# Kernel tuning notes

Hardware: AMD Instinct MI355X
Metric: run time of the kernel (lower is better)

## Reference

```python
import math
import jax, jax.numpy as jnp
import numpy as np

N_NODES = 50000
N_EDGES = 800000
F_IN = 512
HID = 64
N_CLS = 64
NITER = 10


def setup_inputs() -> dict:
    key = jax.random.key(0)
    k = jax.random.split(key, 6)
    x = jax.random.normal(k[0], (N_NODES, F_IN), jnp.float32)
    edge_index = jax.random.randint(k[1], (2, N_EDGES), 0, N_NODES, jnp.int64)
    W1 = jax.random.normal(k[2], (F_IN, HID), jnp.float32) / np.sqrt(F_IN)
    b1 = jnp.zeros((HID,), jnp.float32)
    W2 = jax.random.normal(k[3], (HID, N_CLS), jnp.float32) / np.sqrt(HID)
    b2 = jnp.zeros((N_CLS,), jnp.float32)
    halt_w = jax.random.normal(k[4], (N_CLS,), jnp.float32) / np.sqrt(N_CLS)
    # reset_parameters: bias = log((1/(niter+1)) / (1 - 1/(niter+1)))
    b = math.log((1.0 / (NITER + 1)) / (1.0 - 1.0 / (NITER + 1)))
    halt_b = jnp.full((1,), b, jnp.float32)
    return {"x": x, "edge_index": edge_index, "W1": W1, "b1": b1,
            "W2": W2, "b2": b2, "halt_w": halt_w, "halt_b": halt_b}


def reference(x, edge_index, W1, b1, W2, b2, halt_w, halt_b):
    N = x.shape[0]
    # MLP (eval mode: dropout is identity)
    h = jnp.maximum(x @ W1 + b1, 0.0)
    local = h @ W2 + b2                      # [N, C] local predictions
    # GCN normalization with self-loops (eval: no edge dropout)
    loops = jnp.arange(N, dtype=edge_index.dtype)
    row = jnp.concatenate([edge_index[0], loops])
    col = jnp.concatenate([edge_index[1], loops])
    deg = jnp.zeros((N,), x.dtype).at[row].add(1.0)
    dis = jnp.where(deg > 0, jax.lax.rsqrt(jnp.maximum(deg, 1.0)), 0.0)
    norm = dis[row] * dis[col]               # [E+N]

    def step(carry, _):
        prop, steps, sum_h, cont, xacc = carry
        old = prop
        msg = norm[:, None] * prop[row]                       # gather + scale
        prop = jax.ops.segment_sum(msg, col, num_segments=N)  # scatter-add
        hh = jax.nn.sigmoid(prop @ halt_w + halt_b[0])        # [N]
        prob = (sum_h + hh < 0.99) & cont
        pf = prob.astype(x.dtype)
        steps = steps + pf
        sum_h = sum_h + pf * hh
        cond = prob & (steps < NITER)
        p = jnp.where(cond, sum_h, 1.0 - sum_h)
        xacc = xacc + (prop * p[:, None] + old * (1.0 - p)[:, None]) * cont.astype(x.dtype)[:, None]
        cont = cont & prob
        return (prop, steps, sum_h, cont, xacc), None

    init = (local, jnp.ones((N,), x.dtype), jnp.zeros((N,), x.dtype),
            jnp.ones((N,), bool), jnp.zeros_like(local))
    (prop, steps, sum_h, cont, xacc), _ = jax.lax.scan(step, init, None, length=NITER)
    out = xacc / steps[:, None]
    return jax.nn.log_softmax(out, axis=1), steps, 1.0 - sum_h
```

## Files before the change

### kernel.cpp

```cpp
#include <hip/hip_runtime.h>
#include <hip/hip_bf16.h>

#define F_IN 512
#define NC 64
#define NITER 10
#define BM 128
#define BK 64

__global__ __launch_bounds__(256) void init_state_kernel(
    float* __restrict__ steps, float* __restrict__ sumh, int* __restrict__ cont,
    int* __restrict__ rowptr, int N, int E) {
  int i = blockIdx.x * blockDim.x + threadIdx.x;
  if (i < N) { steps[i] = 1.0f; sumh[i] = 0.0f; cont[i] = 1; }
  if (i == 0) rowptr[N] = E;
}

__global__ __launch_bounds__(256) void mlp_kernel(
    const float* __restrict__ x, const float* __restrict__ W1,
    const float* __restrict__ b1, const float* __restrict__ W2,
    const float* __restrict__ b2, float* __restrict__ out, int N) {
  __shared__ float xT[BK * 128];
  __shared__ float ws[BK * NC];
  const int tid  = threadIdx.x;
  const int brow = blockIdx.x * BM;
  const int r0 = (tid >> 4) * 8;
  const int c0 = (tid & 15) * 4;

  float acc[8][4];
#pragma unroll
  for (int j = 0; j < 4; ++j) {
    float bv = b1[c0 + j];
#pragma unroll
    for (int i = 0; i < 8; ++i) acc[i][j] = bv;
  }

  for (int kt = 0; kt < F_IN; kt += BK) {
#pragma unroll
    for (int q = 0; q < 8; ++q) {
      int fidx = q * 256 + tid;
      int row = fidx >> 4, kq = fidx & 15;
      int gr = brow + row; if (gr >= N) gr = N - 1;
      float4 v = *reinterpret_cast<const float4*>(&x[(size_t)gr * F_IN + kt + kq * 4]);
      float vv[4] = {v.x, v.y, v.z, v.w};
#pragma unroll
      for (int j = 0; j < 4; ++j) {
        int kk = kq * 4 + j;
        xT[kk * 128 + (row ^ (kk & 28))] = vv[j];
      }
    }
#pragma unroll
    for (int q = 0; q < 4; ++q) {
      int fidx = q * 256 + tid;
      int row = fidx >> 4, kq = fidx & 15;
      *reinterpret_cast<float4*>(&ws[row * NC + kq * 4]) =
          *reinterpret_cast<const float4*>(&W1[(size_t)(kt + row) * NC + kq * 4]);
    }
    __syncthreads();
#pragma unroll 4
    for (int k = 0; k < BK; ++k) {
      float4 xa = *reinterpret_cast<const float4*>(&xT[k * 128 + (r0 ^ (k & 28))]);
      float4 xb = *reinterpret_cast<const float4*>(&xT[k * 128 + ((r0 + 4) ^ (k & 28))]);
      float4 wv = *reinterpret_cast<const float4*>(&ws[k * NC + c0]);
      float xr[8] = {xa.x, xa.y, xa.z, xa.w, xb.x, xb.y, xb.z, xb.w};
      float wr[4] = {wv.x, wv.y, wv.z, wv.w};
#pragma unroll
      for (int i = 0; i < 8; ++i)
#pragma unroll
        for (int j = 0; j < 4; ++j) acc[i][j] = fmaf(xr[i], wr[j], acc[i][j]);
    }
    __syncthreads();
  }

#pragma unroll
  for (int i = 0; i < 8; ++i)
#pragma unroll
    for (int j = 0; j < 4; ++j) {
      int kk = c0 + j;
      int r  = r0 + i;
      xT[kk * 128 + (r ^ (kk & 28))] = fmaxf(acc[i][j], 0.0f);
    }
#pragma unroll
  for (int q = 0; q < 4; ++q) {
    int fidx = q * 256 + tid;
    int row = fidx >> 4, kq = fidx & 15;
    *reinterpret_cast<float4*>(&ws[row * NC + kq * 4]) =
        *reinterpret_cast<const float4*>(&W2[(size_t)row * NC + kq * 4]);
  }
  float acc2[8][4];
#pragma unroll
  for (int j = 0; j < 4; ++j) {
    float bv = b2[c0 + j];
#pragma unroll
    for (int i = 0; i < 8; ++i) acc2[i][j] = bv;
  }
  __syncthreads();
#pragma unroll 4
  for (int k = 0; k < NC; ++k) {
    float4 xa = *reinterpret_cast<const float4*>(&xT[k * 128 + (r0 ^ (k & 28))]);
    float4 xb = *reinterpret_cast<const float4*>(&xT[k * 128 + ((r0 + 4) ^ (k & 28))]);
    float4 wv = *reinterpret_cast<const float4*>(&ws[k * NC + c0]);
    float xr[8] = {xa.x, xa.y, xa.z, xa.w, xb.x, xb.y, xb.z, xb.w};
    float wr[4] = {wv.x, wv.y, wv.z, wv.w};
#pragma unroll
    for (int i = 0; i < 8; ++i)
#pragma unroll
      for (int j = 0; j < 4; ++j) acc2[i][j] = fmaf(xr[i], wr[j], acc2[i][j]);
  }
#pragma unroll
  for (int i = 0; i < 8; ++i) {
    int gr = brow + r0 + i;
    if (gr < N) {
      float4 o = make_float4(acc2[i][0], acc2[i][1], acc2[i][2], acc2[i][3]);
      *reinterpret_cast<float4*>(&out[(size_t)gr * NC + c0]) = o;
    }
  }
}

__global__ __launch_bounds__(256) void hist_kernel(
    const int* __restrict__ ei, int* __restrict__ deg_i,
    int* __restrict__ indeg, int E) {
  int e = blockIdx.x * blockDim.x + threadIdx.x;
  if (e < E) {
    atomicAdd(&deg_i[ei[e]], 1);
    atomicAdd(&indeg[ei[E + e]], 1);
  }
}

__global__ __launch_bounds__(256) void dis_kernel(
    const int* __restrict__ deg_i, float* __restrict__ dis, int N) {
  int i = blockIdx.x * blockDim.x + threadIdx.x;
  if (i < N) dis[i] = 1.0f / sqrtf((float)(deg_i[i] + 1));
}

__global__ __launch_bounds__(256) void scan_sum_kernel(
    const int* __restrict__ indeg, int* __restrict__ bsum, int N) {
  __shared__ int sm[256];
  int tid = threadIdx.x;
  int i = blockIdx.x * 256 + tid;
  sm[tid] = (i < N) ? indeg[i] : 0;
  __syncthreads();
  for (int s = 128; s > 0; s >>= 1) {
    if (tid < s) sm[tid] += sm[tid + s];
    __syncthreads();
  }
  if (tid == 0) bsum[blockIdx.x] = sm[0];
}

__global__ __launch_bounds__(256) void scan_bsum_kernel(int* __restrict__ bsum, int nb) {
  __shared__ int sm[256];
  int tid = threadIdx.x;
  int v = (tid < nb) ? bsum[tid] : 0;
  sm[tid] = v;
  __syncthreads();
  for (int s = 1; s < 256; s <<= 1) {
    int t = (tid >= s) ? sm[tid - s] : 0;
    __syncthreads();
    sm[tid] += t;
    __syncthreads();
  }
  if (tid < nb) bsum[tid] = sm[tid] - v;
}

__global__ __launch_bounds__(256) void scan_final_kernel(
    const int* __restrict__ indeg, const int* __restrict__ bsum,
    int* __restrict__ rowptr, int N) {
  __shared__ int sm[256];
  int tid = threadIdx.x;
  int i = blockIdx.x * 256 + tid;
  int v = (i < N) ? indeg[i] : 0;
  sm[tid] = v;
  __syncthreads();
  for (int s = 1; s < 256; s <<= 1) {
    int t = (tid >= s) ? sm[tid - s] : 0;
    __syncthreads();
    sm[tid] += t;
    __syncthreads();
  }
  if (i < N) rowptr[i] = bsum[blockIdx.x] + sm[tid] - v;
}

__global__ __launch_bounds__(256) void scatter_kernel(
    const int* __restrict__ ei, const int* __restrict__ rowptr,
    int* __restrict__ cursor, const float* __restrict__ dis,
    int2* __restrict__ csr, int E) {
  int e = blockIdx.x * blockDim.x + threadIdx.x;
  if (e < E) {
    int s = ei[e];
    int c = ei[E + e];
    int pos = rowptr[c] + atomicAdd(&cursor[c], 1);
    csr[pos] = make_int2(s, __float_as_int(dis[s] * dis[c]));
  }
}

__global__ __launch_bounds__(256) void prop_step_kernel(
    const float* __restrict__ prop, float* __restrict__ prop_new,
    const int2* __restrict__ csr, const int* __restrict__ rowptr,
    const float* __restrict__ dis, const float* __restrict__ hw,
    const float* __restrict__ hb, float* __restrict__ steps,
    float* __restrict__ sumh, int* __restrict__ cont,
    float* __restrict__ xacc, int N) {
  int wid = (int)((blockIdx.x * blockDim.x + threadIdx.x) >> 6);
  if (wid >= N) return;
  int lane = threadIdx.x & 63;
  size_t rowoff = (size_t)wid * NC + lane;

  float oldv = prop[rowoff];
  float dc = dis[wid];
  int beg = __builtin_amdgcn_readfirstlane(rowptr[wid]);
  int end = __builtin_amdgcn_readfirstlane(rowptr[wid + 1]);

  float a[8];
  a[0] = dc * dc * oldv;
#pragma unroll
  for (int u = 1; u < 8; ++u) a[u] = 0.0f;
  int i = beg;
  for (; i + 8 <= end; i += 8) {
    int2 e[8];
#pragma unroll
    for (int u = 0; u < 8; ++u) e[u] = csr[i + u];
#pragma unroll
    for (int u = 0; u < 8; ++u)
      a[u] = fmaf(__int_as_float(e[u].y), prop[(size_t)e[u].x * NC + lane], a[u]);
  }
  for (; i < end; ++i) {
    int2 e0 = csr[i];
    a[0] = fmaf(__int_as_float(e0.y), prop[(size_t)e0.x * NC + lane], a[0]);
  }
  float acc = ((a[0] + a[1]) + (a[2] + a[3])) + ((a[4] + a[5]) + (a[6] + a[7]));
  prop_new[rowoff] = acc;

  float z = acc * hw[lane];
#pragma unroll
  for (int off = 32; off > 0; off >>= 1) z += __shfl_xor(z, off);
  z += hb[0];
  float hh = 1.0f / (1.0f + expf(-z));

  float st = steps[wid], sh = sumh[wid];
  int ct = cont[wid];
  bool prob = ((sh + hh) < 0.99f) && (ct != 0);
  float pf = prob ? 1.0f : 0.0f;
  st += pf;
  sh += pf * hh;
  bool cond = prob && (st < (float)NITER);
  float pp = cond ? sh : (1.0f - sh);
  float ctf = ct ? 1.0f : 0.0f;
  xacc[rowoff] += (acc * pp + oldv * (1.0f - pp)) * ctf;
  if (lane == 0) { steps[wid] = st; sumh[wid] = sh; cont[wid] = prob ? 1 : 0; }
}

__global__ __launch_bounds__(256) void final_kernel(
    const float* __restrict__ xacc, const float* __restrict__ steps,
    const float* __restrict__ sumh, float* __restrict__ out0,
    float* __restrict__ out1, float* __restrict__ out2, int N) {
  int wid = (int)((blockIdx.x * blockDim.x + threadIdx.x) >> 6);
  if (wid >= N) return;
  int lane = threadIdx.x & 63;
  float st = steps[wid];
  float v = xacc[(size_t)wid * NC + lane] / st;
  float m = v;
#pragma unroll
  for (int off = 32; off > 0; off >>= 1) m = fmaxf(m, __shfl_xor(m, off));
  float e = expf(v - m);
  float s = e;
#pragma unroll
  for (int off = 32; off > 0; off >>= 1) s += __shfl_xor(s, off);
  out0[(size_t)wid * NC + lane] = v - m - logf(s);
  if (lane == 0) { out1[wid] = st; out2[wid] = 1.0f - sumh[wid]; }
}

extern "C" void kernel_launch(void* const* d_in, const int* in_sizes, int n_in,
                              void* d_out, int out_size, void* d_ws, size_t ws_size,
                              hipStream_t stream) {
  const float* x      = (const float*)d_in[0];
  const int*   ei     = (const int*)d_in[1];
  const float* W1     = (const float*)d_in[2];
  const float* b1     = (const float*)d_in[3];
  const float* W2     = (const float*)d_in[4];
  const float* b2     = (const float*)d_in[5];
  const float* halt_w = (const float*)d_in[6];
  const float* halt_b = (const float*)d_in[7];

  const int N = in_sizes[0] / F_IN;
  const int E = in_sizes[1] / 2;

  char* p = (char*)d_ws;
  auto alloc = [&](size_t bytes) {
    void* r = (void*)p;
    p += (bytes + 255) & ~(size_t)255;
    return r;
  };
  float* propA  = (float*)alloc((size_t)N * NC * 4);
  float* propB  = (float*)alloc((size_t)N * NC * 4);
  float* xacc   = (float*)alloc((size_t)N * NC * 4);
  int2*  csr    = (int2*)alloc((size_t)E * 8);
  int*   rowptr = (int*)alloc((size_t)(N + 1) * 4);
  int*   deg_i  = (int*)alloc((size_t)N * 4);
  int*   indeg  = (int*)alloc((size_t)N * 4);
  int*   cursor = (int*)alloc((size_t)N * 4);
  float* dis    = (float*)alloc((size_t)N * 4);
  float* steps  = (float*)alloc((size_t)N * 4);
  float* sumh   = (float*)alloc((size_t)N * 4);
  int*   cont   = (int*)alloc((size_t)N * 4);
  int*   bsum   = (int*)alloc(1024);

  hipMemsetAsync(deg_i,  0, (size_t)N * 4, stream);
  hipMemsetAsync(indeg,  0, (size_t)N * 4, stream);
  hipMemsetAsync(cursor, 0, (size_t)N * 4, stream);
  hipMemsetAsync(xacc,   0, (size_t)N * NC * 4, stream);

  const int nbN = (N + 255) / 256;
  const int nbE = (E + 255) / 256;
  const int nbM = (N + BM - 1) / BM;

  init_state_kernel<<<nbN, 256, 0, stream>>>(steps, sumh, cont, rowptr, N, E);
  mlp_kernel<<<nbM, 256, 0, stream>>>(x, W1, b1, W2, b2, propA, N);
  hist_kernel<<<nbE, 256, 0, stream>>>(ei, deg_i, indeg, E);
  dis_kernel<<<nbN, 256, 0, stream>>>(deg_i, dis, N);
  scan_sum_kernel<<<nbN, 256, 0, stream>>>(indeg, bsum, N);
  scan_bsum_kernel<<<1, 256, 0, stream>>>(bsum, nbN);
  scan_final_kernel<<<nbN, 256, 0, stream>>>(indeg, bsum, rowptr, N);
  scatter_kernel<<<nbE, 256, 0, stream>>>(ei, rowptr, cursor, dis, csr, E);

  float* out0 = (float*)d_out;
  float* out1 = out0 + (size_t)N * NC;
  float* out2 = out1 + N;

  const float* cur = propA;
  float* nxt = propB;
  const int nbW = (N + 3) / 4;
  for (int it = 0; it < NITER; ++it) {
    prop_step_kernel<<<nbW, 256, 0, stream>>>(cur, nxt, csr, rowptr, dis,
                                              halt_w, halt_b, steps, sumh,
                                              cont, xacc, N);
    const float* t = nxt; nxt = (float*)cur; cur = t;
  }
  final_kernel<<<nbW, 256, 0, stream>>>(xacc, steps, sumh, out0, out1, out2, N);
}
```

Measured before the change: 578.6 us.

## Fuse propagation iterations into one cooperative persistent kernel with grid sync

Replaces the ten per-iteration propagation launches and the final kernel with a single cooperative kernel. Each of 1024 blocks owns 49 nodes, keeps their halting state and accumulator in shared memory, and uses grid.sync between iterations. The goal is to remove launch overhead and global round-trips for steps, sumh, cont and xacc, at the cost of grid-wide barriers and a fixed grid size. It also halves the MLP tile height to 64 rows so more blocks are launched. If the cooperative launch fails, it falls back to the old path.

```diff
diff --git a/kernel.cpp b/kernel.cpp
--- a/kernel.cpp
+++ b/kernel.cpp
@@ -1,11 +1,16 @@
 #include <hip/hip_runtime.h>
 #include <hip/hip_bf16.h>
+#include <hip/hip_cooperative_groups.h>
+
+namespace cg = cooperative_groups;
 
 #define F_IN 512
 #define NC 64
 #define NITER 10
-#define BM 128
+#define BM 64
 #define BK 64
+#define G_COOP 1024
+#define NPB 49
 
 __global__ __launch_bounds__(256) void init_state_kernel(
     float* __restrict__ steps, float* __restrict__ sumh, int* __restrict__ cont,
@@ -19,24 +24,24 @@
     const float* __restrict__ x, const float* __restrict__ W1,
     const float* __restrict__ b1, const float* __restrict__ W2,
     const float* __restrict__ b2, float* __restrict__ out, int N) {
-  __shared__ float xT[BK * 128];
+  __shared__ float xT[BK * BM];
   __shared__ float ws[BK * NC];
   const int tid  = threadIdx.x;
   const int brow = blockIdx.x * BM;
-  const int r0 = (tid >> 4) * 8;
+  const int r0 = (tid >> 4) * 4;
   const int c0 = (tid & 15) * 4;
 
-  float acc[8][4];
+  float acc[4][4];
 #pragma unroll
   for (int j = 0; j < 4; ++j) {
     float bv = b1[c0 + j];
 #pragma unroll
-    for (int i = 0; i < 8; ++i) acc[i][j] = bv;
+    for (int i = 0; i < 4; ++i) acc[i][j] = bv;
   }
 
   for (int kt = 0; kt < F_IN; kt += BK) {
 #pragma unroll
-    for (int q = 0; q < 8; ++q) {
+    for (int q = 0; q < 4; ++q) {
       int fidx = q * 256 + tid;
       int row = fidx >> 4, kq = fidx & 15;
       int gr = brow + row; if (gr >= N) gr = N - 1;
@@ -45,7 +50,7 @@
 #pragma unroll
       for (int j = 0; j < 4; ++j) {
         int kk = kq * 4 + j;
-        xT[kk * 128 + (row ^ (kk & 28))] = vv[j];
+        xT[kk * BM + (row ^ (kk & 28))] = vv[j];
       }
     }
 #pragma unroll
@@ -56,15 +61,14 @@
           *reinterpret_cast<const float4*>(&W1[(size_t)(kt + row) * NC + kq * 4]);
     }
     __syncthreads();
-#pragma unroll 4
+#pragma unroll 8
     for (int k = 0; k < BK; ++k) {
-      float4 xa = *reinterpret_cast<const float4*>(&xT[k * 128 + (r0 ^ (k & 28))]);
-      float4 xb = *reinterpret_cast<const float4*>(&xT[k * 128 + ((r0 + 4) ^ (k & 28))]);
+      float4 xa = *reinterpret_cast<const float4*>(&xT[k * BM + (r0 ^ (k & 28))]);
       float4 wv = *reinterpret_cast<const float4*>(&ws[k * NC + c0]);
-      float xr[8] = {xa.x, xa.y, xa.z, xa.w, xb.x, xb.y, xb.z, xb.w};
+      float xr[4] = {xa.x, xa.y, xa.z, xa.w};
       float wr[4] = {wv.x, wv.y, wv.z, wv.w};
 #pragma unroll
-      for (int i = 0; i < 8; ++i)
+      for (int i = 0; i < 4; ++i)
 #pragma unroll
         for (int j = 0; j < 4; ++j) acc[i][j] = fmaf(xr[i], wr[j], acc[i][j]);
     }
@@ -72,12 +76,12 @@
   }
 
 #pragma unroll
-  for (int i = 0; i < 8; ++i)
+  for (int i = 0; i < 4; ++i)
 #pragma unroll
     for (int j = 0; j < 4; ++j) {
       int kk = c0 + j;
       int r  = r0 + i;
-      xT[kk * 128 + (r ^ (kk & 28))] = fmaxf(acc[i][j], 0.0f);
+      xT[kk * BM + (r ^ (kk & 28))] = fmaxf(acc[i][j], 0.0f);
     }
 #pragma unroll
   for (int q = 0; q < 4; ++q) {
@@ -86,28 +90,27 @@
     *reinterpret_cast<float4*>(&ws[row * NC + kq * 4]) =
         *reinterpret_cast<const float4*>(&W2[(size_t)row * NC + kq * 4]);
   }
-  float acc2[8][4];
+  float acc2[4][4];
 #pragma unroll
   for (int j = 0; j < 4; ++j) {
     float bv = b2[c0 + j];
 #pragma unroll
-    for (int i = 0; i < 8; ++i) acc2[i][j] = bv;
-  }
-  __syncthreads();
-#pragma unroll 4
+    for (int i = 0; i < 4; ++i) acc2[i][j] = bv;
+  }
+  __syncthreads();
+#pragma unroll 8
   for (int k = 0; k < NC; ++k) {
-    float4 xa = *reinterpret_cast<const float4*>(&xT[k * 128 + (r0 ^ (k & 28))]);
-    float4 xb = *reinterpret_cast<const float4*>(&xT[k * 128 + ((r0 + 4) ^ (k & 28))]);
+    float4 xa = *reinterpret_cast<const float4*>(&xT[k * BM + (r0 ^ (k & 28))]);
     float4 wv = *reinterpret_cast<const float4*>(&ws[k * NC + c0]);
-    float xr[8] = {xa.x, xa.y, xa.z, xa.w, xb.x, xb.y, xb.z, xb.w};
+    float xr[4] = {xa.x, xa.y, xa.z, xa.w};
     float wr[4] = {wv.x, wv.y, wv.z, wv.w};
 #pragma unroll
-    for (int i = 0; i < 8; ++i)
+    for (int i = 0; i < 4; ++i)
 #pragma unroll
       for (int j = 0; j < 4; ++j) acc2[i][j] = fmaf(xr[i], wr[j], acc2[i][j]);
   }
 #pragma unroll
-  for (int i = 0; i < 8; ++i) {
+  for (int i = 0; i < 4; ++i) {
     int gr = brow + r0 + i;
     if (gr < N) {
       float4 o = make_float4(acc2[i][0], acc2[i][1], acc2[i][2], acc2[i][3]);
@@ -189,6 +192,110 @@
     int c = ei[E + e];
     int pos = rowptr[c] + atomicAdd(&cursor[c], 1);
     csr[pos] = make_int2(s, __float_as_int(dis[s] * dis[c]));
+  }
+}
+
+__global__ __launch_bounds__(256, 4) void prop_all_kernel(
+    float* __restrict__ bufA, float* __restrict__ bufB,
+    const int2* __restrict__ csr, const int* __restrict__ rowptr,
+    const float* __restrict__ dis, const float* __restrict__ hw,
+    const float* __restrict__ hb,
+    float* __restrict__ out0, float* __restrict__ out1,
+    float* __restrict__ out2, int N) {
+  cg::grid_group grid = cg::this_grid();
+  __shared__ float accrow[NPB][NC];
+  __shared__ float xach[NPB][NC];
+  __shared__ float stA[NPB], shA[NPB], dcA[NPB];
+  __shared__ int ctA[NPB], begA[NPB], endA[NPB];
+
+  const int wv = threadIdx.x >> 6;
+  const int lane = threadIdx.x & 63;
+  const int base = blockIdx.x * NPB;
+  const float hwl = hw[lane];
+  const float hb0 = hb[0];
+
+  for (int j = wv; j < NPB; j += 4) {
+    int node = base + j;
+    if (node < N) {
+      accrow[j][lane] = bufA[(size_t)node * NC + lane];
+      xach[j][lane] = 0.0f;
+      if (lane == 0) {
+        stA[j] = 1.0f; shA[j] = 0.0f; ctA[j] = 1;
+        dcA[j] = dis[node];
+        begA[j] = rowptr[node];
+        endA[j] = rowptr[node + 1];
+      }
+    }
+  }
+  __syncthreads();
+
+  const float* cur = bufA;
+  float* nxt = bufB;
+  for (int it = 0; it < NITER; ++it) {
+    if (it) grid.sync();
+    for (int j = wv; j < NPB; j += 4) {
+      int node = base + j;
+      if (node >= N) continue;
+      float oldv = accrow[j][lane];
+      float dc = dcA[j];
+      int beg = begA[j], iend = endA[j];
+      float a[8];
+      a[0] = dc * dc * oldv;
+#pragma unroll
+      for (int u = 1; u < 8; ++u) a[u] = 0.0f;
+      int i = beg;
+      for (; i + 8 <= iend; i += 8) {
+        int2 e[8];
+#pragma unroll
+        for (int u = 0; u < 8; ++u) e[u] = csr[i + u];
+#pragma unroll
+        for (int u = 0; u < 8; ++u)
+          a[u] = fmaf(__int_as_float(e[u].y), cur[(size_t)e[u].x * NC + lane], a[u]);
+      }
+      for (; i < iend; ++i) {
+        int2 e0 = csr[i];
+        a[0] = fmaf(__int_as_float(e0.y), cur[(size_t)e0.x * NC + lane], a[0]);
+      }
+      float acc = ((a[0] + a[1]) + (a[2] + a[3])) + ((a[4] + a[5]) + (a[6] + a[7]));
+      nxt[(size_t)node * NC + lane] = acc;
+      accrow[j][lane] = acc;
+
+      float z = acc * hwl;
+#pragma unroll
+      for (int off = 32; off > 0; off >>= 1) z += __shfl_xor(z, off);
+      z += hb0;
+      float hh = 1.0f / (1.0f + expf(-z));
+
+      float st = stA[j], sh = shA[j];
+      int ct = ctA[j];
+      bool prob = ((sh + hh) < 0.99f) && (ct != 0);
+      float pf = prob ? 1.0f : 0.0f;
+      st += pf;
+      sh += pf * hh;
+      bool cond = prob && (st < (float)NITER);
+      float pp = cond ? sh : (1.0f - sh);
+      float ctf = ct ? 1.0f : 0.0f;
+      xach[j][lane] += (acc * pp + oldv * (1.0f - pp)) * ctf;
+      if (lane == 0) { stA[j] = st; shA[j] = sh; ctA[j] = prob ? 1 : 0; }
+    }
+    { const float* t = nxt; nxt = (float*)cur; cur = t; }
+  }
+  __syncthreads();
+
+  for (int j = wv; j < NPB; j += 4) {
+    int node = base + j;
+    if (node >= N) continue;
+    float st = stA[j];
+    float v = xach[j][lane] / st;
+    float m = v;
+#pragma unroll
+    for (int off = 32; off > 0; off >>= 1) m = fmaxf(m, __shfl_xor(m, off));
+    float e = expf(v - m);
+    float s = e;
+#pragma unroll
+    for (int off = 32; off > 0; off >>= 1) s += __shfl_xor(s, off);
+    out0[(size_t)node * NC + lane] = v - m - logf(s);
+    if (lane == 0) { out1[node] = st; out2[node] = 1.0f - shA[j]; }
   }
 }
 
@@ -325,14 +432,29 @@
   float* out1 = out0 + (size_t)N * NC;
   float* out2 = out1 + N;
 
-  const float* cur = propA;
-  float* nxt = propB;
-  const int nbW = (N + 3) / 4;
-  for (int it = 0; it < NITER; ++it) {
-    prop_step_kernel<<<nbW, 256, 0, stream>>>(cur, nxt, csr, rowptr, dis,
-                                              halt_w, halt_b, steps, sumh,
-                                              cont, xacc, N);
-    const float* t = nxt; nxt = (float*)cur; cur = t;
-  }
-  final_kernel<<<nbW, 256, 0, stream>>>(xacc, steps, sumh, out0, out1, out2, N);
-}
+  float* bA = propA;
+  float* bB = propB;
+  const int2* csrc = csr;
+  const int* rpc = rowptr;
+  const float* disc = dis;
+  const float* hwc = halt_w;
+  const float* hbc = halt_b;
+  int Nc = N;
+  void* kargs[11] = {&bA, &bB, &csrc, &rpc, &disc, &hwc, &hbc,
+                     &out0, &out1, &out2, &Nc};
+  hipError_t ce = hipLaunchCooperativeKernel(
+      (const void*)prop_all_kernel, dim3(G_COOP), dim3(256), kargs, 0, stream);
+
+  if (ce != hipSuccess) {
+    const float* cur = propA;
+    float* nxt = propB;
+    const int nbW = (N + 3) / 4;
+    for (int it = 0; it < NITER; ++it) {
+      prop_step_kernel<<<nbW, 256, 0, stream>>>(cur, nxt, csr, rowptr, dis,
+                                                halt_w, halt_b, steps, sumh,
+                                                cont, xacc, N);
+      const float* t = nxt; nxt = (float*)cur; cur = t;
+    }
+    final_kernel<<<nbW, 256, 0, stream>>>(xacc, steps, sumh, out0, out1, out2, N);
+  }
+}
```

Result: slower. 1.923 ms (+232.3%).
